# Optimization experiments

Hardware: AMD Instinct MI355X
Metric: run time of the kernel (lower is better)

Reference implementation:

```python
import jax, jax.numpy as jnp
import numpy as np
import math

D_MODEL = 1024
N_HEADS = 16
GEOM_DIM = 7
B, S = 4, 1024


def setup_inputs() -> dict:
    key = jax.random.key(0)
    ks = jax.random.split(key, 12)
    w = lambda k, shape: (jax.random.normal(k, shape, dtype=jnp.float32) * 0.02)
    return {
        "x": jax.random.normal(ks[0], (B, S, D_MODEL), dtype=jnp.float32),
        "geom_feat": jax.random.normal(ks[1], (B, S, S, GEOM_DIM), dtype=jnp.float32),
        "mask": jax.random.randint(ks[2], (B, S), 0, 2, dtype=jnp.int32),
        "Wq": w(ks[3], (D_MODEL, D_MODEL)), "bq": jnp.zeros((D_MODEL,), jnp.float32),
        "Wk": w(ks[4], (D_MODEL, D_MODEL)), "bk": jnp.zeros((D_MODEL,), jnp.float32),
        "Wv": w(ks[5], (D_MODEL, D_MODEL)), "bv": jnp.zeros((D_MODEL,), jnp.float32),
        "Wo": w(ks[6], (D_MODEL, D_MODEL)), "bo": jnp.zeros((D_MODEL,), jnp.float32),
        "Wg": w(ks[7], (GEOM_DIM, N_HEADS)), "bg": jnp.zeros((N_HEADS,), jnp.float32),
    }


def reference(x, geom_feat, mask, Wq, bq, Wk, bk, Wv, bv, Wo, bo, Wg, bg):
    b, s, d = x.shape
    h = Wg.shape[1]
    dk = d // h
    scale = math.sqrt(dk)
    # QKV projections -> [b, h, s, dk]
    Q = (x @ Wq + bq).reshape(b, s, h, dk).transpose(0, 2, 1, 3)
    K = (x @ Wk + bk).reshape(b, s, h, dk).transpose(0, 2, 1, 3)
    V = (x @ Wv + bv).reshape(b, s, h, dk).transpose(0, 2, 1, 3)
    # attention scores [b, h, s, s]
    scores = jnp.einsum("bhqd,bhkd->bhqk", Q, K) / scale
    # geometric structure bias: [b,s,s,geom_dim] -> [b,s,s,h] -> [b,h,s,s]
    struct_bias = (geom_feat @ Wg + bg).transpose(0, 3, 1, 2)
    scores = scores + struct_bias
    # key-padding mask [b, s] -> [b, 1, 1, s]
    scores = jnp.where(mask[:, None, None, :] == 0, -10000.0, scores)
    attn = jax.nn.softmax(scores, axis=-1)  # dropout disabled (eval / p=0)
    ctx = jnp.einsum("bhqk,bhkd->bhqd", attn, V)
    ctx = ctx.transpose(0, 2, 1, 3).reshape(b, s, d)
    return ctx @ Wo + bo
```

## Files before the change

### kernel.cpp

```cpp
#include <hip/hip_runtime.h>
#include <hip/hip_bf16.h>
#include <math.h>

#define BB 4
#define SS 1024
#define DD 1024
#define NH 16
#define DK 64
#define GD 7

typedef _Float16 half8 __attribute__((ext_vector_type(8)));
typedef _Float16 half4v __attribute__((ext_vector_type(4)));
typedef float floatx4 __attribute__((ext_vector_type(4)));

__device__ __forceinline__ void async_cp16(const void* g, void* l) {
  __builtin_amdgcn_global_load_lds(
      (const __attribute__((address_space(1))) void*)g,
      (__attribute__((address_space(3))) void*)l, 16, 0, 0);
}

__device__ inline half8 cvt8(const float4 a, const float4 b) {
  half8 h;
  h[0] = (_Float16)a.x; h[1] = (_Float16)a.y; h[2] = (_Float16)a.z; h[3] = (_Float16)a.w;
  h[4] = (_Float16)b.x; h[5] = (_Float16)b.y; h[6] = (_Float16)b.z; h[7] = (_Float16)b.w;
  return h;
}

__global__ __launch_bounds__(256) void prep(const float* __restrict__ x,
                                            _Float16* __restrict__ xh,
                                            const float* __restrict__ Wq,
                                            const float* __restrict__ Wk,
                                            const float* __restrict__ Wv,
                                            const float* __restrict__ Wo,
                                            _Float16* __restrict__ Wt) {
  __shared__ _Float16 Tl[64 * 72];
  const int t = threadIdx.x;
  if (blockIdx.x < 2048) {
    const int i = blockIdx.x * 256 + t;
    const float4 a = ((const float4*)x)[i * 2];
    const float4 b = ((const float4*)x)[i * 2 + 1];
    ((half8*)xh)[i] = cvt8(a, b);
    return;
  }
  const int pf = blockIdx.x - 2048;
  const int z = pf >> 8, rem = pf & 255;
  const int n0 = (rem >> 4) * 64, k0 = (rem & 15) * 64;
  const float* src = (z == 0) ? Wq : (z == 1) ? Wk : (z == 2) ? Wv : Wo;
#pragma unroll
  for (int i = 0; i < 4; ++i) {
    const int u = i * 256 + t;
    const int r = u >> 4, c4 = (u & 15) * 4;
    const float4 v = *(const float4*)(src + (size_t)(k0 + r) * DD + n0 + c4);
    Tl[(c4 + 0) * 72 + r] = (_Float16)v.x;
    Tl[(c4 + 1) * 72 + r] = (_Float16)v.y;
    Tl[(c4 + 2) * 72 + r] = (_Float16)v.z;
    Tl[(c4 + 3) * 72 + r] = (_Float16)v.w;
  }
  __syncthreads();
  _Float16* dst = Wt + (size_t)z * DD * DD;
#pragma unroll
  for (int i = 0; i < 2; ++i) {
    const int u = i * 256 + t;
    const int nr = u >> 3, ks = u & 7;
    const half8 hv = *(const half8*)&Tl[nr * 72 + ks * 8];
    *(half8*)(dst + (size_t)(n0 + nr) * DD + k0 + ks * 8) = hv;
  }
}

__global__ __launch_bounds__(256) void gemmQKV(const _Float16* __restrict__ A,
                                               const _Float16* __restrict__ Bt,
                                               const float* __restrict__ bq,
                                               const float* __restrict__ bk,
                                               const float* __restrict__ bv,
                                               _Float16* __restrict__ Oq,
                                               _Float16* __restrict__ Ok,
                                               _Float16* __restrict__ Ov) {
  __shared__ _Float16 Als[128 * 64];
  __shared__ _Float16 Bls[128 * 64];
  const int t = threadIdx.x;
  const int raw = blockIdx.x;
  const int idx = (raw & 7) * 96 + (raw >> 3);
  const int w = t >> 6, lane = t & 63, quad = lane >> 4, col = lane & 15;
  const int m0 = (idx & 31) * 128, n0 = (idx >> 5) * 128;
  const int mw = (w >> 1) * 64, nw = (w & 1) * 64;
  const int lr = lane >> 3, ls = lane & 7;
  const int swz8 = (ls ^ lr) * 8;
  const floatx4 zero4 = {0.f, 0.f, 0.f, 0.f};
  floatx4 acc[4][4];
#pragma unroll
  for (int i = 0; i < 4; ++i)
#pragma unroll
    for (int j = 0; j < 4; ++j) acc[i][j] = zero4;

  const _Float16* aBase = A + (size_t)(m0 + lr) * DD + swz8;
  const _Float16* bBase = Bt + (size_t)(n0 + lr) * DD + swz8;

  for (int k0 = 0; k0 < DD; k0 += 64) {
#pragma unroll
    for (int it = 0; it < 4; ++it) {
      const int rb = it * 32 + w * 8;
      async_cp16(aBase + (size_t)rb * DD + k0, &Als[rb * 64]);
      async_cp16(bBase + (size_t)rb * DD + k0, &Bls[rb * 64]);
    }
    __syncthreads();
#pragma unroll
    for (int kk = 0; kk < 2; ++kk) {
      half8 af[4], bf[4];
      const int sz = ((quad + kk * 4) ^ (col & 7)) * 8;
#pragma unroll
      for (int i = 0; i < 4; ++i)
        af[i] = *(const half8*)&Als[(mw + i * 16 + col) * 64 + sz];
#pragma unroll
      for (int j = 0; j < 4; ++j)
        bf[j] = *(const half8*)&Bls[(nw + j * 16 + col) * 64 + sz];
#pragma unroll
      for (int i = 0; i < 4; ++i)
#pragma unroll
        for (int j = 0; j < 4; ++j)
          acc[i][j] =
              __builtin_amdgcn_mfma_f32_16x16x32_f16(af[i], bf[j], acc[i][j], 0, 0, 0);
    }
    __syncthreads();
  }

#pragma unroll
  for (int j = 0; j < 4; ++j) {
    const int n = n0 + nw + j * 16 + col;
    const int which = n >> 10, hd = n & 1023;
    const int h = hd >> 6, d = hd & 63;
    const float* bp = (which == 0) ? bq : (which == 1) ? bk : bv;
    const float bias = bp[hd];
    _Float16* ob = (which == 0) ? Oq : (which == 1) ? Ok : Ov;
#pragma unroll
    for (int i = 0; i < 4; ++i) {
#pragma unroll
      for (int reg = 0; reg < 4; ++reg) {
        const int m = m0 + mw + i * 16 + quad * 4 + reg;
        const int b = m >> 10, s = m & 1023;
        ob[(((size_t)b * NH + h) * SS + s) * DK + d] = (_Float16)(acc[i][j][reg] + bias);
      }
    }
  }
}

__global__ __launch_bounds__(256) void biasprep(const float* __restrict__ geom,
                                                const int* __restrict__ mask,
                                                const float* __restrict__ Wg,
                                                const float* __restrict__ bg,
                                                unsigned char* __restrict__ bias8) {
  __shared__ float wgL[GD * NH + NH];
  const int t = threadIdx.x;
  const int r = blockIdx.x;
  const int b = r >> 9;
  const int q = (r & 511) * 2 + (t >> 7);
  const int k8 = (t & 127) * 8;
  if (t < GD * NH) wgL[t] = Wg[t];
  if (t < NH) wgL[GD * NH + t] = bg[t];

  const float* gp = geom + ((size_t)b * SS + q) * SS * GD + (size_t)k8 * GD;
  float4 gv[14];
#pragma unroll
  for (int i = 0; i < 14; ++i) gv[i] = *(const float4*)(gp + i * 4);
  const float* gf = (const float*)gv;

  const int4 m4a = *(const int4*)(mask + b * SS + k8);
  const int4 m4b = *(const int4*)(mask + b * SS + k8 + 4);
  const int mk[8] = {m4a.x, m4a.y, m4a.z, m4a.w, m4b.x, m4b.y, m4b.z, m4b.w};

  __syncthreads();

  unsigned char* dst = bias8 + ((size_t)b * NH * SS + q) * SS + k8;
#pragma unroll
  for (int h = 0; h < NH; ++h) {
    float wg[GD];
#pragma unroll
    for (int g = 0; g < GD; ++g) wg[g] = wgL[g * NH + h];
    const float bgh = wgL[GD * NH + h];
    float bi[8];
#pragma unroll
    for (int k2 = 0; k2 < 8; ++k2) {
      float s = bgh;
#pragma unroll
      for (int g = 0; g < GD; ++g) s = fmaf(gf[k2 * GD + g], wg[g], s);
      bi[k2] = mk[k2] ? s : -100.f;
    }
    int w0 = 0, w1 = 0;
    w0 = __builtin_amdgcn_cvt_pk_fp8_f32(bi[0], bi[1], w0, false);
    w0 = __builtin_amdgcn_cvt_pk_fp8_f32(bi[2], bi[3], w0, true);
    w1 = __builtin_amdgcn_cvt_pk_fp8_f32(bi[4], bi[5], w1, false);
    w1 = __builtin_amdgcn_cvt_pk_fp8_f32(bi[6], bi[7], w1, true);
    uint2 u2v;
    u2v.x = (unsigned)w0;
    u2v.y = (unsigned)w1;
    *(uint2*)(dst + (size_t)h * SS * SS) = u2v;
  }
}

__global__ __launch_bounds__(256) void hgemm1(const _Float16* __restrict__ A,
                                              const _Float16* __restrict__ Bt,
                                              const float* __restrict__ b0,
                                              float* __restrict__ Of) {
  __shared__ _Float16 Als[128 * 64];
  __shared__ _Float16 Bls[128 * 64];
  const int t = threadIdx.x;
  const int w = t >> 6, lane = t & 63, quad = lane >> 4, col = lane & 15;
  const int m0 = blockIdx.x * 128, n0 = blockIdx.y * 128;
  const int mw = (w >> 1) * 64, nw = (w & 1) * 64;
  const int lr = lane >> 3, ls = lane & 7;
  const int swz8 = (ls ^ lr) * 8;
  const floatx4 zero4 = {0.f, 0.f, 0.f, 0.f};
  floatx4 acc[4][4];
#pragma unroll
  for (int i = 0; i < 4; ++i)
#pragma unroll
    for (int j = 0; j < 4; ++j) acc[i][j] = zero4;

  const _Float16* aBase = A + (size_t)(m0 + lr) * DD + swz8;
  const _Float16* bBase = Bt + (size_t)(n0 + lr) * DD + swz8;

  for (int k0 = 0; k0 < DD; k0 += 64) {
#pragma unroll
    for (int it = 0; it < 4; ++it) {
      const int rb = it * 32 + w * 8;
      async_cp16(aBase + (size_t)rb * DD + k0, &Als[rb * 64]);
      async_cp16(bBase + (size_t)rb * DD + k0, &Bls[rb * 64]);
    }
    __syncthreads();
#pragma unroll
    for (int kk = 0; kk < 2; ++kk) {
      half8 af[4], bf[4];
      const int sz = ((quad + kk * 4) ^ (col & 7)) * 8;
#pragma unroll
      for (int i = 0; i < 4; ++i) af[i] = *(const half8*)&Als[(mw + i * 16 + col) * 64 + sz];
#pragma unroll
      for (int j = 0; j < 4; ++j) bf[j] = *(const half8*)&Bls[(nw + j * 16 + col) * 64 + sz];
#pragma unroll
      for (int i = 0; i < 4; ++i)
#pragma unroll
        for (int j = 0; j < 4; ++j)
          acc[i][j] = __builtin_amdgcn_mfma_f32_16x16x32_f16(af[i], bf[j], acc[i][j], 0, 0, 0);
    }
    __syncthreads();
  }

#pragma unroll
  for (int j = 0; j < 4; ++j) {
    const int n = n0 + nw + j * 16 + col;
    const float bias = b0[n];
#pragma unroll
    for (int i = 0; i < 4; ++i) {
#pragma unroll
      for (int reg = 0; reg < 4; ++reg) {
        const int m = m0 + mw + i * 16 + quad * 4 + reg;
        Of[(size_t)m * DD + n] = acc[i][j][reg] + bias;
      }
    }
  }
}

__global__ __launch_bounds__(256) void attnP(const _Float16* __restrict__ Q,
                                             const _Float16* __restrict__ K,
                                             const _Float16* __restrict__ V,
                                             const unsigned char* __restrict__ bias8,
                                             _Float16* __restrict__ ctxbuf) {
  __shared__ _Float16 Qs[64 * 64];
  __shared__ _Float16 Ks[2][64 * 64];
  __shared__ _Float16 Vt[64 * 72];
  __shared__ unsigned char biasL[64 * 80];

  const int t = threadIdx.x;
  const int w = t >> 6, lane = t & 63, quad = lane >> 4, col = lane & 15;
  const int h = blockIdx.x, qt = blockIdx.y, b = blockIdx.z;
  const int q0 = qt * 64;
  const size_t bh = (size_t)b * NH + h;
  const _Float16* Qb = Q + bh * SS * DK;
  const _Float16* Kb = K + bh * SS * DK;
  const _Float16* Vb = V + bh * SS * DK;
  const unsigned char* bb8 = bias8 + (bh * SS + q0) * SS;

  const int lr = lane >> 3, ls = lane & 7;
  const int swz8 = (ls ^ lr) * 8;

  const int kg = (t >> 4) * 4, dg = (t & 15) * 4;
  const int cg = (kg & 0x20) | ((kg & 0x0C) << 1) | ((kg & 0x10) >> 2);
  const int brow = t >> 2, bseg = (t & 3) * 16;

#pragma unroll
  for (int it = 0; it < 2; ++it) {
    const int rb = it * 32 + w * 8;
    async_cp16(Qb + (size_t)(q0 + rb + lr) * DK + swz8, &Qs[rb * 64]);
  }
#pragma unroll
  for (int it = 0; it < 2; ++it) {
    const int rb = it * 32 + w * 8;
    async_cp16(Kb + (size_t)(rb + lr) * DK + swz8, &Ks[0][rb * 64]);
  }
  half4v vreg[4];
#pragma unroll
  for (int e = 0; e < 4; ++e)
    vreg[e] = *(const half4v*)(Vb + (size_t)(kg + e) * DK + dg);
  uint4 breg = *(const uint4*)(bb8 + (size_t)brow * SS + bseg);

  __syncthreads();
  half8 qfrag[2];
  {
    const int qrow = w * 16 + col;
#pragma unroll
    for (int kk = 0; kk < 2; ++kk)
      qfrag[kk] = *(const half8*)&Qs[qrow * 64 + (((quad + kk * 4) ^ (col & 7)) * 8)];
  }

  const floatx4 zero4 = {0.f, 0.f, 0.f, 0.f};
  floatx4 ctx[4] = {zero4, zero4, zero4, zero4};
  float lsum = 0.f;

  for (int c = 0; c < 16; ++c) {
    const int cur = c & 1;
    __syncthreads();

    if (c < 15) {
#pragma unroll
      for (int it = 0; it < 2; ++it) {
        const int rb = it * 32 + w * 8;
        async_cp16(Kb + (size_t)((c + 1) * 64 + rb + lr) * DK + swz8,
                   &Ks[cur ^ 1][rb * 64]);
      }
    }
#pragma unroll
    for (int i = 0; i < 4; ++i) {
      half4v hv = {vreg[0][i], vreg[1][i], vreg[2][i], vreg[3][i]};
      *(half4v*)&Vt[(dg + i) * 72 + cg] = hv;
    }
    *(uint4*)&biasL[brow * 80 + bseg] = breg;

    asm volatile("s_waitcnt lgkmcnt(0)" ::: "memory");
    __builtin_amdgcn_s_barrier();
    __builtin_amdgcn_sched_barrier(0);

    if (c < 15) {
      const int kn = (c + 1) * 64;
#pragma unroll
      for (int e = 0; e < 4; ++e)
        vreg[e] = *(const half4v*)(Vb + (size_t)(kn + kg + e) * DK + dg);
      breg = *(const uint4*)(bb8 + (size_t)brow * SS + kn + bseg);
    }
    __builtin_amdgcn_sched_barrier(0);

    floatx4 sc[4] = {zero4, zero4, zero4, zero4};
#pragma unroll
    for (int nt = 0; nt < 4; ++nt) {
      const int key = nt * 16 + col;
#pragma unroll
      for (int kk = 0; kk < 2; ++kk) {
        const half8 kf =
            *(const half8*)&Ks[cur][key * 64 + (((quad + kk * 4) ^ (col & 7)) * 8)];
        sc[nt] = __builtin_amdgcn_mfma_f32_16x16x32_f16(kf, qfrag[kk], sc[nt], 0, 0, 0);
      }
    }

    float ps[4][4];
#pragma unroll
    for (int nt = 0; nt < 4; ++nt) {
      const unsigned bw =
          *(const unsigned*)&biasL[(w * 16 + col) * 80 + nt * 16 + quad * 4];
      float bias4[4];
      bias4[0] = __builtin_amdgcn_cvt_f32_fp8((int)bw, 0);
      bias4[1] = __builtin_amdgcn_cvt_f32_fp8((int)bw, 1);
      bias4[2] = __builtin_amdgcn_cvt_f32_fp8((int)bw, 2);
      bias4[3] = __builtin_amdgcn_cvt_f32_fp8((int)bw, 3);
#pragma unroll
      for (int reg = 0; reg < 4; ++reg) {
        const float s = fmaf(sc[nt][reg], 0.125f, bias4[reg]);
        const float p = __expf(s);
        lsum += p;
        ps[nt][reg] = p;
      }
    }

#pragma unroll
    for (int kk = 0; kk < 2; ++kk) {
      half8 pf;
      pf[0] = (_Float16)ps[2 * kk][0];
      pf[1] = (_Float16)ps[2 * kk][1];
      pf[2] = (_Float16)ps[2 * kk][2];
      pf[3] = (_Float16)ps[2 * kk][3];
      pf[4] = (_Float16)ps[2 * kk + 1][0];
      pf[5] = (_Float16)ps[2 * kk + 1][1];
      pf[6] = (_Float16)ps[2 * kk + 1][2];
      pf[7] = (_Float16)ps[2 * kk + 1][3];
#pragma unroll
      for (int nt = 0; nt < 4; ++nt) {
        const half8 vb = *(const half8*)&Vt[(nt * 16 + col) * 72 + quad * 8 + kk * 32];
        ctx[nt] = __builtin_amdgcn_mfma_f32_16x16x32_f16(vb, pf, ctx[nt], 0, 0, 0);
      }
    }
  }

  float l = lsum;
  l += __shfl_xor(l, 16, 64);
  l += __shfl_xor(l, 32, 64);
  const float inv = 1.f / l;

  _Float16* op = ctxbuf + ((size_t)b * SS + q0 + w * 16 + col) * DD + h * DK + quad * 4;
#pragma unroll
  for (int nt = 0; nt < 4; ++nt) {
    half4v o;
#pragma unroll
    for (int reg = 0; reg < 4; ++reg) o[reg] = (_Float16)(ctx[nt][reg] * inv);
    *(half4v*)(op + nt * 16) = o;
  }
}

__global__ __launch_bounds__(256) void attnF(const _Float16* __restrict__ Q,
                                             const _Float16* __restrict__ K,
                                             const _Float16* __restrict__ V,
                                             const float* __restrict__ geom,
                                             const int* __restrict__ mask,
                                             const float* __restrict__ Wg,
                                             const float* __restrict__ bg,
                                             _Float16* __restrict__ ctxbuf) {
  __shared__ _Float16 Ks[64 * 64];
  __shared__ _Float16 Vt[64 * 72];
  __shared__ _Float16 biasLf[64 * 72];
  __shared__ unsigned char mskL[SS];

  const int t = threadIdx.x;
  const int w = t >> 6, lane = t & 63, quad = lane >> 4, col = lane & 15;
  const int h = blockIdx.x, qt = blockIdx.y, b = blockIdx.z;
  const int q0 = qt * 64;
  const size_t bh = (size_t)b * NH + h;
  const _Float16* Qb = Q + bh * SS * DK;
  const _Float16* Kb = K + bh * SS * DK;
  const _Float16* Vb = V + bh * SS * DK;

  const int lr = lane >> 3, ls = lane & 7;
  const int swz8 = (ls ^ lr) * 8;

#pragma unroll
  for (int it = 0; it < 2; ++it) {
    const int rb = it * 32 + w * 8;
    async_cp16(Qb + (size_t)(q0 + rb + lr) * DK + swz8, &Ks[rb * 64]);
  }
  {
    const int4 m4 = *(const int4*)(mask + b * SS + t * 4);
    mskL[t * 4 + 0] = m4.x != 0;
    mskL[t * 4 + 1] = m4.y != 0;
    mskL[t * 4 + 2] = m4.z != 0;
    mskL[t * 4 + 3] = m4.w != 0;
  }
  __syncthreads();
  half8 qfrag[2];
  {
    const int qrow = w * 16 + col;
#pragma unroll
    for (int kk = 0; kk < 2; ++kk)
      qfrag[kk] = *(const half8*)&Ks[qrow * 64 + (((quad + kk * 4) ^ (col & 7)) * 8)];
  }

  float wgv[GD];
#pragma unroll
  for (int g = 0; g < GD; ++g) wgv[g] = Wg[g * NH + h];
  const float bgh = bg[h];
  const float* gptr = geom + (((size_t)b * SS + (q0 + (t >> 2))) * SS + (t & 3) * 16) * GD;

  const floatx4 zero4 = {0.f, 0.f, 0.f, 0.f};
  floatx4 ctx[4] = {zero4, zero4, zero4, zero4};
  float lsum = 0.f;

  const int kg = (t >> 4) * 4, dg = (t & 15) * 4;
  const int cg = (kg & 0x20) | ((kg & 0x0C) << 1) | ((kg & 0x10) >> 2);

  for (int c = 0; c < 16; ++c) {
    const int k0c = c * 64;
    __syncthreads();

#pragma unroll
    for (int it = 0; it < 2; ++it) {
      const int rb = it * 32 + w * 8;
      async_cp16(Kb + (size_t)(k0c + rb + lr) * DK + swz8, &Ks[rb * 64]);
    }
    {
      half4v f[4];
#pragma unroll
      for (int e = 0; e < 4; ++e)
        f[e] = *(const half4v*)(Vb + (size_t)(k0c + kg + e) * DK + dg);
#pragma unroll
      for (int i = 0; i < 4; ++i) {
        half4v hv = {f[0][i], f[1][i], f[2][i], f[3][i]};
        *(half4v*)&Vt[(dg + i) * 72 + cg] = hv;
      }
    }
    {
      const int gq = t >> 2, gk = (t & 3) * 16;
#pragma unroll
      for (int sg = 0; sg < 4; ++sg) {
        float4 gvv[7];
#pragma unroll
        for (int i7 = 0; i7 < 7; ++i7) gvv[i7] = *(const float4*)(gptr + sg * 28 + i7 * 4);
        const float* gf = (const float*)gvv;
        half4v bv;
#pragma unroll
        for (int k2 = 0; k2 < 4; ++k2) {
          float bi = bgh;
#pragma unroll
          for (int g = 0; g < GD; ++g) bi = fmaf(gf[k2 * GD + g], wgv[g], bi);
          bv[k2] = mskL[k0c + gk + sg * 4 + k2] ? (_Float16)bi : (_Float16)(-100.f);
        }
        *(half4v*)&biasLf[gq * 72 + gk + sg * 4] = bv;
      }
      gptr += 64 * GD;
    }
    __syncthreads();

    floatx4 sc[4] = {zero4, zero4, zero4, zero4};
#pragma unroll
    for (int nt = 0; nt < 4; ++nt) {
      const int key = nt * 16 + col;
#pragma unroll
      for (int kk = 0; kk < 2; ++kk) {
        const half8 kf = *(const half8*)&Ks[key * 64 + (((quad + kk * 4) ^ (col & 7)) * 8)];
        sc[nt] = __builtin_amdgcn_mfma_f32_16x16x32_f16(kf, qfrag[kk], sc[nt], 0, 0, 0);
      }
    }

    float ps[4][4];
#pragma unroll
    for (int nt = 0; nt < 4; ++nt) {
#pragma unroll
      for (int reg = 0; reg < 4; ++reg) {
        const float bias = (float)biasLf[(w * 16 + col) * 72 + nt * 16 + quad * 4 + reg];
        const float s = fmaf(sc[nt][reg], 0.125f, bias);
        const float p = __expf(s);
        lsum += p;
        ps[nt][reg] = p;
      }
    }

#pragma unroll
    for (int kk = 0; kk < 2; ++kk) {
      half8 pf;
      pf[0] = (_Float16)ps[2 * kk][0];
      pf[1] = (_Float16)ps[2 * kk][1];
      pf[2] = (_Float16)ps[2 * kk][2];
      pf[3] = (_Float16)ps[2 * kk][3];
      pf[4] = (_Float16)ps[2 * kk + 1][0];
      pf[5] = (_Float16)ps[2 * kk + 1][1];
      pf[6] = (_Float16)ps[2 * kk + 1][2];
      pf[7] = (_Float16)ps[2 * kk + 1][3];
#pragma unroll
      for (int nt = 0; nt < 4; ++nt) {
        const half8 vb = *(const half8*)&Vt[(nt * 16 + col) * 72 + quad * 8 + kk * 32];
        ctx[nt] = __builtin_amdgcn_mfma_f32_16x16x32_f16(vb, pf, ctx[nt], 0, 0, 0);
      }
    }
  }

  float l = lsum;
  l += __shfl_xor(l, 16, 64);
  l += __shfl_xor(l, 32, 64);
  const float inv = 1.f / l;

  _Float16* op = ctxbuf + ((size_t)b * SS + q0 + w * 16 + col) * DD + h * DK + quad * 4;
#pragma unroll
  for (int nt = 0; nt < 4; ++nt) {
    half4v o;
#pragma unroll
    for (int reg = 0; reg < 4; ++reg) o[reg] = (_Float16)(ctx[nt][reg] * inv);
    *(half4v*)(op + nt * 16) = o;
  }
}

extern "C" void kernel_launch(void* const* d_in, const int* in_sizes, int n_in,
                              void* d_out, int out_size, void* d_ws, size_t ws_size,
                              hipStream_t stream) {
  const float* x    = (const float*)d_in[0];
  const float* geom = (const float*)d_in[1];
  const int*   mask = (const int*)d_in[2];
  const float* Wq   = (const float*)d_in[3];
  const float* bq   = (const float*)d_in[4];
  const float* Wk   = (const float*)d_in[5];
  const float* bk   = (const float*)d_in[6];
  const float* Wv   = (const float*)d_in[7];
  const float* bv   = (const float*)d_in[8];
  const float* Wo   = (const float*)d_in[9];
  const float* bo   = (const float*)d_in[10];
  const float* Wg   = (const float*)d_in[11];
  const float* bg   = (const float*)d_in[12];
  float* out = (float*)d_out;

  const size_t NEL = (size_t)BB * SS * DD;
  char* p = (char*)d_ws;
  _Float16* xh   = (_Float16*)p;            p += NEL * 2;
  _Float16* Wt   = (_Float16*)p;            p += NEL * 2;
  _Float16* Qh   = (_Float16*)p;            p += NEL * 2;
  _Float16* Kh   = (_Float16*)p;            p += NEL * 2;
  _Float16* Vh   = (_Float16*)p;            p += NEL * 2;
  _Float16* ctxh = (_Float16*)p;            p += NEL * 2;
  unsigned char* bias8 = (unsigned char*)p;
  const size_t need = (size_t)48 * 1024 * 1024 + (size_t)BB * NH * SS * SS;
  const bool prebias = ws_size >= need;

  prep<<<3072, 256, 0, stream>>>(x, xh, Wq, Wk, Wv, Wo, Wt);
  gemmQKV<<<768, 256, 0, stream>>>(xh, Wt, bq, bk, bv, Qh, Kh, Vh);

  if (prebias) {
    biasprep<<<2048, 256, 0, stream>>>(geom, mask, Wg, bg, bias8);
    attnP<<<dim3(NH, SS / 64, BB), 256, 0, stream>>>(Qh, Kh, Vh, bias8, ctxh);
  } else {
    attnF<<<dim3(NH, SS / 64, BB), 256, 0, stream>>>(Qh, Kh, Vh, geom, mask, Wg, bg, ctxh);
  }

  hgemm1<<<dim3(32, 8), 256, 0, stream>>>(ctxh, Wt + (size_t)3 * DD * DD, bo, out);
}
```

Before: 332.2 us.

## Fuse bias precompute into prep kernel and restructure attention pipeline

Merges the geometric-bias precompute into the fp16 conversion/transpose prep kernel, interleaving block roles so the memory-bound bias pass overlaps the weight and activation conversion and one launch is saved. In attnP, Q fragments are read straight from global instead of being staged through LDS. The K double buffer is split into two named arrays, the loop is unrolled by two with a bias prefetch two chunks ahead, and the grid is reordered so consecutive blocks share a head. This trades some register pressure and bias load pattern for fewer barriers, a smaller LDS footprint and better cache locality.

```diff
diff --git a/kernel.cpp b/kernel.cpp
--- a/kernel.cpp
+++ b/kernel.cpp
@@ -26,44 +26,112 @@
   return h;
 }
 
-__global__ __launch_bounds__(256) void prep(const float* __restrict__ x,
-                                            _Float16* __restrict__ xh,
-                                            const float* __restrict__ Wq,
-                                            const float* __restrict__ Wk,
-                                            const float* __restrict__ Wv,
-                                            const float* __restrict__ Wo,
-                                            _Float16* __restrict__ Wt) {
+template <bool PRE>
+__global__ __launch_bounds__(256) void prep2(const float* __restrict__ x,
+                                             _Float16* __restrict__ xh,
+                                             const float* __restrict__ Wq,
+                                             const float* __restrict__ Wk,
+                                             const float* __restrict__ Wv,
+                                             const float* __restrict__ Wo,
+                                             _Float16* __restrict__ Wt,
+                                             const float* __restrict__ geom,
+                                             const int* __restrict__ mask,
+                                             const float* __restrict__ Wg,
+                                             const float* __restrict__ bg,
+                                             unsigned char* __restrict__ bias8) {
   __shared__ _Float16 Tl[64 * 72];
+  __shared__ float wgL[GD * NH + NH];
   const int t = threadIdx.x;
-  if (blockIdx.x < 2048) {
-    const int i = blockIdx.x * 256 + t;
+  int role, idx;
+  if (PRE) {
+    const int grp = blockIdx.x / 5, rem = blockIdx.x % 5;
+    if (rem < 2)      { role = 0; idx = grp * 2 + rem; }
+    else if (rem < 4) { role = 1; idx = grp * 2 + rem - 2; }
+    else              { role = 2; idx = grp; }
+  } else {
+    role = (blockIdx.x < 2048) ? 1 : 2;
+    idx = (role == 1) ? blockIdx.x : blockIdx.x - 2048;
+  }
+
+  if (role == 1) {
+    const int i = idx * 256 + t;
     const float4 a = ((const float4*)x)[i * 2];
     const float4 b = ((const float4*)x)[i * 2 + 1];
     ((half8*)xh)[i] = cvt8(a, b);
     return;
   }
-  const int pf = blockIdx.x - 2048;
-  const int z = pf >> 8, rem = pf & 255;
-  const int n0 = (rem >> 4) * 64, k0 = (rem & 15) * 64;
-  const float* src = (z == 0) ? Wq : (z == 1) ? Wk : (z == 2) ? Wv : Wo;
-#pragma unroll
-  for (int i = 0; i < 4; ++i) {
-    const int u = i * 256 + t;
-    const int r = u >> 4, c4 = (u & 15) * 4;
-    const float4 v = *(const float4*)(src + (size_t)(k0 + r) * DD + n0 + c4);
-    Tl[(c4 + 0) * 72 + r] = (_Float16)v.x;
-    Tl[(c4 + 1) * 72 + r] = (_Float16)v.y;
-    Tl[(c4 + 2) * 72 + r] = (_Float16)v.z;
-    Tl[(c4 + 3) * 72 + r] = (_Float16)v.w;
-  }
-  __syncthreads();
-  _Float16* dst = Wt + (size_t)z * DD * DD;
-#pragma unroll
-  for (int i = 0; i < 2; ++i) {
-    const int u = i * 256 + t;
-    const int nr = u >> 3, ks = u & 7;
-    const half8 hv = *(const half8*)&Tl[nr * 72 + ks * 8];
-    *(half8*)(dst + (size_t)(n0 + nr) * DD + k0 + ks * 8) = hv;
+
+  if (role == 2) {
+    const int z = idx >> 8, rem2 = idx & 255;
+    const int n0 = (rem2 >> 4) * 64, k0 = (rem2 & 15) * 64;
+    const float* src = (z == 0) ? Wq : (z == 1) ? Wk : (z == 2) ? Wv : Wo;
+#pragma unroll
+    for (int i = 0; i < 4; ++i) {
+      const int u = i * 256 + t;
+      const int r = u >> 4, c4 = (u & 15) * 4;
+      const float4 v = *(const float4*)(src + (size_t)(k0 + r) * DD + n0 + c4);
+      Tl[(c4 + 0) * 72 + r] = (_Float16)v.x;
+      Tl[(c4 + 1) * 72 + r] = (_Float16)v.y;
+      Tl[(c4 + 2) * 72 + r] = (_Float16)v.z;
+      Tl[(c4 + 3) * 72 + r] = (_Float16)v.w;
+    }
+    __syncthreads();
+    _Float16* dst = Wt + (size_t)z * DD * DD;
+#pragma unroll
+    for (int i = 0; i < 2; ++i) {
+      const int u = i * 256 + t;
+      const int nr = u >> 3, ks = u & 7;
+      const half8 hv = *(const half8*)&Tl[nr * 72 + ks * 8];
+      *(half8*)(dst + (size_t)(n0 + nr) * DD + k0 + ks * 8) = hv;
+    }
+    return;
+  }
+
+  if constexpr (PRE) {
+    const int r = idx;
+    const int b = r >> 9;
+    const int q = (r & 511) * 2 + (t >> 7);
+    const int k8 = (t & 127) * 8;
+    if (t < GD * NH) wgL[t] = Wg[t];
+    if (t < NH) wgL[GD * NH + t] = bg[t];
+
+    const float* gp = geom + ((size_t)b * SS + q) * SS * GD + (size_t)k8 * GD;
+    float4 gv[14];
+#pragma unroll
+    for (int i = 0; i < 14; ++i) gv[i] = *(const float4*)(gp + i * 4);
+    const float* gf = (const float*)gv;
+
+    const int4 m4a = *(const int4*)(mask + b * SS + k8);
+    const int4 m4b = *(const int4*)(mask + b * SS + k8 + 4);
+    const int mk[8] = {m4a.x, m4a.y, m4a.z, m4a.w, m4b.x, m4b.y, m4b.z, m4b.w};
+
+    __syncthreads();
+
+    unsigned char* dst = bias8 + ((size_t)b * NH * SS + q) * SS + k8;
+#pragma unroll
+    for (int h = 0; h < NH; ++h) {
+      float wg[GD];
+#pragma unroll
+      for (int g = 0; g < GD; ++g) wg[g] = wgL[g * NH + h];
+      const float bgh = wgL[GD * NH + h];
+      float bi[8];
+#pragma unroll
+      for (int k2 = 0; k2 < 8; ++k2) {
+        float s = bgh;
+#pragma unroll
+        for (int g = 0; g < GD; ++g) s = fmaf(gf[k2 * GD + g], wg[g], s);
+        bi[k2] = mk[k2] ? s : -100.f;
+      }
+      int w0 = 0, w1 = 0;
+      w0 = __builtin_amdgcn_cvt_pk_fp8_f32(bi[0], bi[1], w0, false);
+      w0 = __builtin_amdgcn_cvt_pk_fp8_f32(bi[2], bi[3], w0, true);
+      w1 = __builtin_amdgcn_cvt_pk_fp8_f32(bi[4], bi[5], w1, false);
+      w1 = __builtin_amdgcn_cvt_pk_fp8_f32(bi[6], bi[7], w1, true);
+      uint2 u2v;
+      u2v.x = (unsigned)w0;
+      u2v.y = (unsigned)w1;
+      *(uint2*)(dst + (size_t)h * SS * SS) = u2v;
+    }
   }
 }
 
@@ -143,59 +211,6 @@
   }
 }
 
-__global__ __launch_bounds__(256) void biasprep(const float* __restrict__ geom,
-                                                const int* __restrict__ mask,
-                                                const float* __restrict__ Wg,
-                                                const float* __restrict__ bg,
-                                                unsigned char* __restrict__ bias8) {
-  __shared__ float wgL[GD * NH + NH];
-  const int t = threadIdx.x;
-  const int r = blockIdx.x;
-  const int b = r >> 9;
-  const int q = (r & 511) * 2 + (t >> 7);
-  const int k8 = (t & 127) * 8;
-  if (t < GD * NH) wgL[t] = Wg[t];
-  if (t < NH) wgL[GD * NH + t] = bg[t];
-
-  const float* gp = geom + ((size_t)b * SS + q) * SS * GD + (size_t)k8 * GD;
-  float4 gv[14];
-#pragma unroll
-  for (int i = 0; i < 14; ++i) gv[i] = *(const float4*)(gp + i * 4);
-  const float* gf = (const float*)gv;
-
-  const int4 m4a = *(const int4*)(mask + b * SS + k8);
-  const int4 m4b = *(const int4*)(mask + b * SS + k8 + 4);
-  const int mk[8] = {m4a.x, m4a.y, m4a.z, m4a.w, m4b.x, m4b.y, m4b.z, m4b.w};
-
-  __syncthreads();
-
-  unsigned char* dst = bias8 + ((size_t)b * NH * SS + q) * SS + k8;
-#pragma unroll
-  for (int h = 0; h < NH; ++h) {
-    float wg[GD];
-#pragma unroll
-    for (int g = 0; g < GD; ++g) wg[g] = wgL[g * NH + h];
-    const float bgh = wgL[GD * NH + h];
-    float bi[8];
-#pragma unroll
-    for (int k2 = 0; k2 < 8; ++k2) {
-      float s = bgh;
-#pragma unroll
-      for (int g = 0; g < GD; ++g) s = fmaf(gf[k2 * GD + g], wg[g], s);
-      bi[k2] = mk[k2] ? s : -100.f;
-    }
-    int w0 = 0, w1 = 0;
-    w0 = __builtin_amdgcn_cvt_pk_fp8_f32(bi[0], bi[1], w0, false);
-    w0 = __builtin_amdgcn_cvt_pk_fp8_f32(bi[2], bi[3], w0, true);
-    w1 = __builtin_amdgcn_cvt_pk_fp8_f32(bi[4], bi[5], w1, false);
-    w1 = __builtin_amdgcn_cvt_pk_fp8_f32(bi[6], bi[7], w1, true);
-    uint2 u2v;
-    u2v.x = (unsigned)w0;
-    u2v.y = (unsigned)w1;
-    *(uint2*)(dst + (size_t)h * SS * SS) = u2v;
-  }
-}
-
 __global__ __launch_bounds__(256) void hgemm1(const _Float16* __restrict__ A,
                                               const _Float16* __restrict__ Bt,
                                               const float* __restrict__ b0,
@@ -263,14 +278,14 @@
                                              const _Float16* __restrict__ V,
                                              const unsigned char* __restrict__ bias8,
                                              _Float16* __restrict__ ctxbuf) {
-  __shared__ _Float16 Qs[64 * 64];
-  __shared__ _Float16 Ks[2][64 * 64];
+  __shared__ _Float16 Ks0[64 * 64];
+  __shared__ _Float16 Ks1[64 * 64];
   __shared__ _Float16 Vt[64 * 72];
   __shared__ unsigned char biasL[64 * 80];
 
   const int t = threadIdx.x;
   const int w = t >> 6, lane = t & 63, quad = lane >> 4, col = lane & 15;
-  const int h = blockIdx.x, qt = blockIdx.y, b = blockIdx.z;
+  const int qt = blockIdx.x, h = blockIdx.y, b = blockIdx.z;
   const int q0 = qt * 64;
   const size_t bh = (size_t)b * NH + h;
   const _Float16* Qb = Q + bh * SS * DK;
@@ -288,42 +303,36 @@
 #pragma unroll
   for (int it = 0; it < 2; ++it) {
     const int rb = it * 32 + w * 8;
-    async_cp16(Qb + (size_t)(q0 + rb + lr) * DK + swz8, &Qs[rb * 64]);
-  }
-#pragma unroll
-  for (int it = 0; it < 2; ++it) {
-    const int rb = it * 32 + w * 8;
-    async_cp16(Kb + (size_t)(rb + lr) * DK + swz8, &Ks[0][rb * 64]);
+    async_cp16(Kb + (size_t)(rb + lr) * DK + swz8, &Ks0[rb * 64]);
   }
   half4v vreg[4];
 #pragma unroll
   for (int e = 0; e < 4; ++e)
     vreg[e] = *(const half4v*)(Vb + (size_t)(kg + e) * DK + dg);
-  uint4 breg = *(const uint4*)(bb8 + (size_t)brow * SS + bseg);
-
-  __syncthreads();
+  uint4 bregA = *(const uint4*)(bb8 + (size_t)brow * SS + bseg);
+  uint4 bregB = *(const uint4*)(bb8 + (size_t)brow * SS + 64 + bseg);
+
   half8 qfrag[2];
   {
     const int qrow = w * 16 + col;
 #pragma unroll
     for (int kk = 0; kk < 2; ++kk)
-      qfrag[kk] = *(const half8*)&Qs[qrow * 64 + (((quad + kk * 4) ^ (col & 7)) * 8)];
+      qfrag[kk] = *(const half8*)(Qb + (size_t)(q0 + qrow) * DK + (quad + kk * 4) * 8);
   }
 
   const floatx4 zero4 = {0.f, 0.f, 0.f, 0.f};
   floatx4 ctx[4] = {zero4, zero4, zero4, zero4};
   float lsum = 0.f;
 
-  for (int c = 0; c < 16; ++c) {
-    const int cur = c & 1;
-    __syncthreads();
-
-    if (c < 15) {
+  auto subchunk = [&](int c_, _Float16* KsC, _Float16* KsN, uint4& brg) {
+    __syncthreads();
+
+    if (c_ < 15) {
 #pragma unroll
       for (int it = 0; it < 2; ++it) {
         const int rb = it * 32 + w * 8;
-        async_cp16(Kb + (size_t)((c + 1) * 64 + rb + lr) * DK + swz8,
-                   &Ks[cur ^ 1][rb * 64]);
+        async_cp16(Kb + (size_t)((c_ + 1) * 64 + rb + lr) * DK + swz8,
+                   &KsN[rb * 64]);
       }
     }
 #pragma unroll
@@ -331,18 +340,19 @@
       half4v hv = {vreg[0][i], vreg[1][i], vreg[2][i], vreg[3][i]};
       *(half4v*)&Vt[(dg + i) * 72 + cg] = hv;
     }
-    *(uint4*)&biasL[brow * 80 + bseg] = breg;
+    *(uint4*)&biasL[brow * 80 + bseg] = brg;
 
     asm volatile("s_waitcnt lgkmcnt(0)" ::: "memory");
     __builtin_amdgcn_s_barrier();
     __builtin_amdgcn_sched_barrier(0);
 
-    if (c < 15) {
-      const int kn = (c + 1) * 64;
+    if (c_ < 15) {
+      const int kn = (c_ + 1) * 64;
 #pragma unroll
       for (int e = 0; e < 4; ++e)
         vreg[e] = *(const half4v*)(Vb + (size_t)(kn + kg + e) * DK + dg);
-      breg = *(const uint4*)(bb8 + (size_t)brow * SS + kn + bseg);
+      const int kb2 = ((c_ + 2 < 16) ? (c_ + 2) : 15) * 64;
+      brg = *(const uint4*)(bb8 + (size_t)brow * SS + kb2 + bseg);
     }
     __builtin_amdgcn_sched_barrier(0);
 
@@ -353,7 +363,7 @@
 #pragma unroll
       for (int kk = 0; kk < 2; ++kk) {
         const half8 kf =
-            *(const half8*)&Ks[cur][key * 64 + (((quad + kk * 4) ^ (col & 7)) * 8)];
+            *(const half8*)&KsC[key * 64 + (((quad + kk * 4) ^ (col & 7)) * 8)];
         sc[nt] = __builtin_amdgcn_mfma_f32_16x16x32_f16(kf, qfrag[kk], sc[nt], 0, 0, 0);
       }
     }
@@ -394,6 +404,11 @@
         ctx[nt] = __builtin_amdgcn_mfma_f32_16x16x32_f16(vb, pf, ctx[nt], 0, 0, 0);
       }
     }
+  };
+
+  for (int cp = 0; cp < 8; ++cp) {
+    subchunk(2 * cp, Ks0, Ks1, bregA);
+    subchunk(2 * cp + 1, Ks1, Ks0, bregB);
   }
 
   float l = lsum;
@@ -600,13 +615,15 @@
   const size_t need = (size_t)48 * 1024 * 1024 + (size_t)BB * NH * SS * SS;
   const bool prebias = ws_size >= need;
 
-  prep<<<3072, 256, 0, stream>>>(x, xh, Wq, Wk, Wv, Wo, Wt);
-  gemmQKV<<<768, 256, 0, stream>>>(xh, Wt, bq, bk, bv, Qh, Kh, Vh);
-
   if (prebias) {
-    biasprep<<<2048, 256, 0, stream>>>(geom, mask, Wg, bg, bias8);
-    attnP<<<dim3(NH, SS / 64, BB), 256, 0, stream>>>(Qh, Kh, Vh, bias8, ctxh);
+    prep2<true><<<5120, 256, 0, stream>>>(x, xh, Wq, Wk, Wv, Wo, Wt,
+                                          geom, mask, Wg, bg, bias8);
+    gemmQKV<<<768, 256, 0, stream>>>(xh, Wt, bq, bk, bv, Qh, Kh, Vh);
+    attnP<<<dim3(SS / 64, NH, BB), 256, 0, stream>>>(Qh, Kh, Vh, bias8, ctxh);
   } else {
+    prep2<false><<<3072, 256, 0, stream>>>(x, xh, Wq, Wk, Wv, Wo, Wt,
+                                           geom, mask, Wg, bg, nullptr);
+    gemmQKV<<<768, 256, 0, stream>>>(xh, Wt, bq, bk, bv, Qh, Kh, Vh);
     attnF<<<dim3(NH, SS / 64, BB), 256, 0, stream>>>(Qh, Kh, Vh, geom, mask, Wg, bg, ctxh);
   }
 
```

Result: no change. 333.5 us (+0.4%).
